# Kernel optimization log

Hardware: AMD Instinct MI355X
Metric: run time of the kernel (lower is better)

## Reference

```python
import jax, jax.numpy as jnp
import numpy as np

B, P, D, H, DH = 2, 2048, 1024, 16, 64
EPS = 1e-5

def layernorm(x, g, b):
    mu = jnp.mean(x, axis=-1, keepdims=True)
    var = jnp.mean((x - mu) ** 2, axis=-1, keepdims=True)
    return (x - mu) * jax.lax.rsqrt(var + EPS) * g + b

def setup_inputs() -> dict:
    key = jax.random.key(0)
    ks = jax.random.split(key, 16)
    s = lambda *sh: 1.0 / np.sqrt(sh[-2] if len(sh) > 1 else sh[-1])
    return {
        "x": jax.random.normal(ks[0], (B, P, D), jnp.float32),
        "Wq": jax.random.normal(ks[1], (H, D, DH), jnp.float32) / np.sqrt(D),
        "Wk": jax.random.normal(ks[2], (H, D, DH), jnp.float32) / np.sqrt(D),
        "Wv": jax.random.normal(ks[3], (H, D, DH), jnp.float32) / np.sqrt(D),
        "Wp": jax.random.normal(ks[4], (D, D), jnp.float32) / np.sqrt(D),
        "bp": jax.random.normal(ks[5], (D,), jnp.float32) * 0.01,
        "W1": jax.random.normal(ks[6], (D, 4 * D), jnp.float32) / np.sqrt(D),
        "b1": jax.random.normal(ks[7], (4 * D,), jnp.float32) * 0.01,
        "W2": jax.random.normal(ks[8], (4 * D, D), jnp.float32) / np.sqrt(4 * D),
        "b2": jax.random.normal(ks[9], (D,), jnp.float32) * 0.01,
        "g1": jnp.ones((D,), jnp.float32),
        "be1": jnp.zeros((D,), jnp.float32),
        "g2": jnp.ones((D,), jnp.float32),
        "be2": jnp.zeros((D,), jnp.float32),
    }

def reference(x, Wq, Wk, Wv, Wp, bp, W1, b1, W2, b2, g1, be1, g2, be2):
    Bb, Pp, Dd = x.shape
    h = layernorm(x, g1, be1)
    # per-head projections, stacked: [B,H,P,DH]
    q = jnp.einsum('bpd,hde->bhpe', h, Wq)
    k = jnp.einsum('bpd,hde->bhpe', h, Wk)
    v = jnp.einsum('bpd,hde->bhpe', h, Wv)
    # NOTE: source scales by dim_embd**-0.5 (C = x.shape[-1]), not dim_head
    scores = jnp.einsum('bhpe,bhqe->bhpq', q, k) * (Dd ** -0.5)
    mask = jnp.tril(jnp.ones((Pp, Pp), bool))
    scores = jnp.where(mask, scores, -jnp.inf)
    att = jax.nn.softmax(scores, axis=-1)
    o = jnp.einsum('bhpq,bhqe->bhpe', att, v)
    # concat heads: [B,P,H*DH]
    o = o.transpose(0, 2, 1, 3).reshape(Bb, Pp, -1)
    x = x + o @ Wp + bp
    h2 = layernorm(x, g2, be2)
    m = jax.nn.gelu(h2 @ W1 + b1, approximate=False)
    x = x + m @ W2 + b2
    return x
```

## Files before the change

### kernel.cpp

```cpp
#include <hip/hip_runtime.h>
#include <hip/hip_bf16.h>
#include <stdint.h>

typedef unsigned short u16;
typedef __attribute__((ext_vector_type(4))) float f32x4;
typedef __attribute__((ext_vector_type(8))) short bf16x8;
typedef __attribute__((ext_vector_type(4))) short bf16x4;
typedef __attribute__((ext_vector_type(4))) unsigned short u16x4;

static __device__ __forceinline__ u16 f2bf(float f) {
    union { float f; unsigned u; } v; v.f = f;
    unsigned r = v.u + 0x7fffu + ((v.u >> 16) & 1u);
    return (u16)(r >> 16);
}

static __device__ __forceinline__ void gload_lds16(const u16* g, u16* l) {
    __builtin_amdgcn_global_load_lds(
        (const __attribute__((address_space(1))) void*)(uintptr_t)g,
        (__attribute__((address_space(3))) void*)(uint32_t)(uintptr_t)l,
        16, 0, 0);
}

__global__ __launch_bounds__(256) void transpose_cast_b(
    const float* __restrict__ W, u16* __restrict__ out,
    int K, int N, long in_bs, long out_bs)
{
    __shared__ float tile[32][33];
    const float* Wb = W + (size_t)blockIdx.z * in_bs;
    u16* ob = out + (size_t)blockIdx.z * out_bs;
    int nt = blockIdx.x * 32, kt = blockIdx.y * 32;
    int tx = threadIdx.x & 31, ty = threadIdx.x >> 5;
    #pragma unroll
    for (int i = ty; i < 32; i += 8)
        tile[i][tx] = Wb[(size_t)(kt + i) * N + nt + tx];
    __syncthreads();
    #pragma unroll
    for (int i = ty; i < 32; i += 8)
        ob[(size_t)(nt + i) * K + kt + tx] = f2bf(tile[tx][i]);
}

__global__ __launch_bounds__(256) void ln_kernel(
    const float* __restrict__ x, const float* __restrict__ g,
    const float* __restrict__ be, u16* __restrict__ out)
{
    int row = blockIdx.x;
    int t = threadIdx.x;
    const float4* xr = (const float4*)(x + (size_t)row * 1024);
    float4 v = xr[t];
    float s = v.x + v.y + v.z + v.w;
    float sq = v.x * v.x + v.y * v.y + v.z * v.z + v.w * v.w;
    #pragma unroll
    for (int o = 1; o < 64; o <<= 1) {
        s  += __shfl_xor(s, o);
        sq += __shfl_xor(sq, o);
    }
    __shared__ float ps[4], pq[4];
    if ((t & 63) == 0) { ps[t >> 6] = s; pq[t >> 6] = sq; }
    __syncthreads();
    float S = ps[0] + ps[1] + ps[2] + ps[3];
    float Q = pq[0] + pq[1] + pq[2] + pq[3];
    float mu = S * (1.0f / 1024.0f);
    float var = Q * (1.0f / 1024.0f) - mu * mu;
    float rs = rsqrtf(var + 1e-5f);
    const float4 g4  = ((const float4*)g)[t];
    const float4 be4 = ((const float4*)be)[t];
    u16x4 o4;
    o4[0] = f2bf((v.x - mu) * rs * g4.x + be4.x);
    o4[1] = f2bf((v.y - mu) * rs * g4.y + be4.y);
    o4[2] = f2bf((v.z - mu) * rs * g4.z + be4.z);
    o4[3] = f2bf((v.w - mu) * rs * g4.w + be4.w);
    *(u16x4*)(out + (size_t)row * 1024 + t * 4) = o4;
}

template<int EPI>
__global__ __launch_bounds__(256) void gemm_bt(
    const u16* __restrict__ A, const u16* __restrict__ Bt,
    int M, int N, int K,
    const float* __restrict__ bias,
    void* __restrict__ Cout, u16* __restrict__ Kf, u16* __restrict__ Vf)
{
    __shared__ __align__(16) u16 SH[32768];
    const int bid = blockIdx.x;
    const int xcd = bid & 7, idx = bid >> 3;
    const int nmx = N >> 7;
    const int spx = (M >> 7) >> 3;
    const int tm = (xcd * spx + idx / nmx) * 128;
    const int tn = (idx % nmx) * 128;
    const int t = threadIdx.x;
    const int lane = t & 63, wave = t >> 6;
    const int wr = wave >> 1, wc = wave & 1;
    const int lq = lane & 15, lg = lane >> 4;
    f32x4 acc[4][4] = {};

    const int srow8 = lane >> 3;
    const int skoff = ((lane & 7) ^ srow8) * 8;
    const u16* ag = A  + (size_t)(tm + wave * 32 + srow8) * K + skoff;
    const u16* bg = Bt + (size_t)(tn + wave * 32 + srow8) * K + skoff;

    auto STAGE = [&](int buf, int k0) {
        u16* ab = SH + buf * 16384 + wave * 2048;
        u16* bb = SH + buf * 16384 + 8192 + wave * 2048;
        #pragma unroll
        for (int j = 0; j < 4; ++j) {
            gload_lds16(ag + (size_t)(j * 8) * K + k0, ab + j * 512);
            gload_lds16(bg + (size_t)(j * 8) * K + k0, bb + j * 512);
        }
    };

    const int KT = K >> 6;
    STAGE(0, 0);
    STAGE(1, 64);
    asm volatile("s_waitcnt vmcnt(8)" ::: "memory");
    __builtin_amdgcn_sched_barrier(0);
    __builtin_amdgcn_s_barrier();

    for (int kt = 0; kt < KT; ++kt) {
        const int buf = kt & 1;
        const u16* abuf = SH + buf * 16384;
        const u16* bbuf = abuf + 8192;
        bf16x8 af[4][2], bfv[4][2];
        #pragma unroll
        for (int m = 0; m < 4; ++m) {
            const int row = wr * 64 + m * 16 + lq;
            #pragma unroll
            for (int kk = 0; kk < 2; ++kk) {
                const int slot = (kk * 4 + lg) ^ (row & 7);
                af[m][kk] = *(const bf16x8*)(abuf + row * 64 + slot * 8);
            }
        }
        #pragma unroll
        for (int n = 0; n < 4; ++n) {
            const int col = wc * 64 + n * 16 + lq;
            #pragma unroll
            for (int kk = 0; kk < 2; ++kk) {
                const int slot = (kk * 4 + lg) ^ (col & 7);
                bfv[n][kk] = *(const bf16x8*)(bbuf + col * 64 + slot * 8);
            }
        }
        asm volatile("s_waitcnt lgkmcnt(0)" ::: "memory");
        __builtin_amdgcn_sched_barrier(0);
        __builtin_amdgcn_s_barrier();

        const bool pre = (kt + 2 < KT);
        if (pre) STAGE(buf, (kt + 2) << 6);

        __builtin_amdgcn_s_setprio(1);
        #pragma unroll
        for (int m = 0; m < 4; ++m)
            #pragma unroll
            for (int n = 0; n < 4; ++n)
                #pragma unroll
                for (int kk = 0; kk < 2; ++kk)
                    acc[m][n] = __builtin_amdgcn_mfma_f32_16x16x32_bf16(
                        af[m][kk], bfv[n][kk], acc[m][n], 0, 0, 0);
        __builtin_amdgcn_s_setprio(0);

        if (kt + 1 < KT) {
            if (pre) asm volatile("s_waitcnt vmcnt(8)" ::: "memory");
            else     asm volatile("s_waitcnt vmcnt(0)" ::: "memory");
            __builtin_amdgcn_sched_barrier(0);
            __builtin_amdgcn_s_barrier();
        }
    }

    if (EPI == 2 || (EPI == 3 && tn < 1024)) {
        __syncthreads();
        #pragma unroll
        for (int n = 0; n < 4; ++n) {
            const int cl = wc * 64 + n * 16 + lq;
            #pragma unroll
            for (int m = 0; m < 4; ++m) {
                const int rl = wr * 64 + m * 16 + lg * 4;
                #pragma unroll
                for (int r = 0; r < 4; ++r) {
                    float v = acc[m][n][r];
                    if (EPI == 2) {
                        float xx = v + bias[tn + cl];
                        v = 0.5f * xx * (1.0f + erff(xx * 0.70710678118654752f));
                    }
                    SH[(rl + r) * 136 + cl] = f2bf(v);
                }
            }
        }
        __syncthreads();
        const int row = t >> 1, half = t & 1;
        const int ncols = (EPI == 2) ? N : 1024;
        const uint4* srow4 = (const uint4*)(SH + row * 136 + half * 64);
        uint4* drow = (uint4*)((u16*)Cout + (size_t)(tm + row) * ncols + tn + half * 64);
        #pragma unroll
        for (int i = 0; i < 8; ++i)
            drow[i] = srow4[i];
    } else if (EPI == 3) {
        __syncthreads();
        const bool isK = (tn < 2048);
        #pragma unroll
        for (int n = 0; n < 4; ++n) {
            const int cl = wc * 64 + n * 16 + lq;
            const int d = cl & 63, hl = cl >> 6;
            #pragma unroll
            for (int m = 0; m < 4; ++m) {
                const int rl0 = wr * 64 + m * 16 + lg * 4;
                #pragma unroll
                for (int r = 0; r < 4; ++r) {
                    const int rl = rl0 + r;
                    const int p = rl & 63, kl = rl >> 6;
                    int off;
                    if (isK)
                        off = ((p >> 4) * 2 + (d >> 5)) * 512 + ((d >> 3) & 3) * 128
                            + (p & 15) * 8 + (d & 7);
                    else
                        off = ((p >> 4) * 4 + (d >> 4)) * 256 + ((p >> 2) & 3) * 64
                            + (d & 15) * 4 + (p & 3);
                    SH[(hl * 2 + kl) * 4096 + off] = f2bf(acc[m][n][r]);
                }
            }
        }
        __syncthreads();
        const int img = t >> 6, ln = t & 63;
        const int hl = img >> 1, kl = img & 1;
        const int hh = ((tn - (isK ? 1024 : 2048)) >> 6) + hl;
        const int bb = tm >> 11, pp = tm & 2047;
        u16* base = (isK ? Kf : Vf) + (size_t)(bb * 16 + hh) * 131072
                  + (size_t)((pp >> 6) + kl) * 4096;
        const u16* simg = SH + img * 4096;
        #pragma unroll
        for (int i = 0; i < 8; ++i)
            *(uint4*)(base + ln * 8 + i * 512) = *(const uint4*)(simg + ln * 8 + i * 512);
    }
}

__global__ __launch_bounds__(256) void gemm_bt64(
    const u16* __restrict__ A, const u16* __restrict__ Bt,
    int M, int N, int K,
    const float* __restrict__ bias, const float* __restrict__ res,
    float* __restrict__ Cout)
{
    __shared__ __align__(16) u16 SH[24576];
    const int bid = blockIdx.x;
    const int xcd = bid & 7, idx = bid >> 3;
    const int nmx = N >> 6;
    const int spx = (M >> 7) >> 3;
    const int tm = (xcd * spx + idx / nmx) * 128;
    const int tn = (idx % nmx) * 64;
    const int t = threadIdx.x;
    const int lane = t & 63, wave = t >> 6;
    const int wr = wave >> 1, wc = wave & 1;
    const int lq = lane & 15, lg = lane >> 4;
    f32x4 acc[4][2] = {};

    const int srow8 = lane >> 3;
    const int skoff = ((lane & 7) ^ srow8) * 8;
    const u16* ag = A  + (size_t)(tm + wave * 32 + srow8) * K + skoff;
    const u16* bg = Bt + (size_t)(tn + wave * 16 + srow8) * K + skoff;

    auto STAGE = [&](int buf, int k0) {
        u16* ab = SH + buf * 12288 + wave * 2048;
        u16* bb = SH + buf * 12288 + 8192 + wave * 1024;
        #pragma unroll
        for (int j = 0; j < 4; ++j)
            gload_lds16(ag + (size_t)(j * 8) * K + k0, ab + j * 512);
        #pragma unroll
        for (int j = 0; j < 2; ++j)
            gload_lds16(bg + (size_t)(j * 8) * K + k0, bb + j * 512);
    };

    const int KT = K >> 6;
    STAGE(0, 0);
    STAGE(1, 64);
    asm volatile("s_waitcnt vmcnt(6)" ::: "memory");
    __builtin_amdgcn_sched_barrier(0);
    __builtin_amdgcn_s_barrier();

    for (int kt = 0; kt < KT; ++kt) {
        const int buf = kt & 1;
        const u16* abuf = SH + buf * 12288;
        const u16* bbuf = abuf + 8192;
        bf16x8 af[4][2], bfr[2][2];
        #pragma unroll
        for (int m = 0; m < 4; ++m) {
            const int row = wr * 64 + m * 16 + lq;
            #pragma unroll
            for (int kk = 0; kk < 2; ++kk) {
                const int slot = (kk * 4 + lg) ^ (row & 7);
                af[m][kk] = *(const bf16x8*)(abuf + row * 64 + slot * 8);
            }
        }
        #pragma unroll
        for (int n = 0; n < 2; ++n) {
            const int col = wc * 32 + n * 16 + lq;
            #pragma unroll
            for (int kk = 0; kk < 2; ++kk) {
                const int slot = (kk * 4 + lg) ^ (col & 7);
                bfr[n][kk] = *(const bf16x8*)(bbuf + col * 64 + slot * 8);
            }
        }
        asm volatile("s_waitcnt lgkmcnt(0)" ::: "memory");
        __builtin_amdgcn_sched_barrier(0);
        __builtin_amdgcn_s_barrier();

        const bool pre = (kt + 2 < KT);
        if (pre) STAGE(buf, (kt + 2) << 6);

        __builtin_amdgcn_s_setprio(1);
        #pragma unroll
        for (int m = 0; m < 4; ++m)
            #pragma unroll
            for (int n = 0; n < 2; ++n)
                #pragma unroll
                for (int kk = 0; kk < 2; ++kk)
                    acc[m][n] = __builtin_amdgcn_mfma_f32_16x16x32_bf16(
                        af[m][kk], bfr[n][kk], acc[m][n], 0, 0, 0);
        __builtin_amdgcn_s_setprio(0);

        if (kt + 1 < KT) {
            if (pre) asm volatile("s_waitcnt vmcnt(6)" ::: "memory");
            else     asm volatile("s_waitcnt vmcnt(0)" ::: "memory");
            __builtin_amdgcn_sched_barrier(0);
            __builtin_amdgcn_s_barrier();
        }
    }

    #pragma unroll
    for (int m = 0; m < 4; ++m)
        #pragma unroll
        for (int n = 0; n < 2; ++n) {
            const int col = tn + wc * 32 + n * 16 + lq;
            #pragma unroll
            for (int r = 0; r < 4; ++r) {
                const int row = tm + wr * 64 + m * 16 + lg * 4 + r;
                Cout[(size_t)row * N + col] = acc[m][n][r] + bias[col] + res[(size_t)row * N + col];
            }
        }
}

__global__ __launch_bounds__(256, 4) void attn_kernel(
    const u16* __restrict__ qb, const u16* __restrict__ Kf,
    const u16* __restrict__ Vf, u16* __restrict__ o)
{
    const int P = 2048;
    __shared__ __align__(16) u16 KB[2][4096];
    __shared__ __align__(16) u16 VB[2][4096];
    int blk = blockIdx.x;
    int qt = 31 - (blk >> 5);
    int bh = blk & 31;
    int h = bh & 15, b = bh >> 4;
    int w = threadIdx.x >> 6, lane = threadIdx.x & 63;
    int lq = lane & 15, lg = lane >> 4;
    int q0 = qt * 64 + w * 16;
    const u16* qptr = qb + (size_t)(b * P + q0 + lq) * 1024 + h * 64 + lg * 8;
    bf16x8 qf0 = *(const bf16x8*)qptr;
    bf16x8 qf1 = *(const bf16x8*)(qptr + 32);
    const u16* Kfb = Kf + (size_t)bh * 131072;
    const u16* Vfb = Vf + (size_t)bh * 131072;
    const float C2 = 0.03125f * 1.44269504f;
    const int moff = w * 16 + lq;
    float m2 = -1e30f, l_run = 0.f;
    f32x4 accO[4] = {};
    const int nkvb = qt + 1;

    const int vsel = w >> 1, half = w & 1;
    auto STAGE = [&](int buf, int kvb) {
        const u16* src = (vsel ? Vfb : Kfb) + (size_t)kvb * 4096 + half * 2048 + lane * 8;
        u16* dst = (vsel ? &VB[buf][half * 2048] : &KB[buf][half * 2048]);
        #pragma unroll
        for (int i = 0; i < 4; ++i)
            gload_lds16(src + i * 512, dst + i * 512);
    };

    auto COMPUTE = [&](int buf, bool last) {
        const u16* kbase = KB[buf] + lane * 8;
        f32x4 st[4];
        #pragma unroll
        for (int ss = 0; ss < 4; ++ss) {
            bf16x8 kf0 = *(const bf16x8*)(kbase + ss * 1024);
            bf16x8 kf1 = *(const bf16x8*)(kbase + ss * 1024 + 512);
            f32x4 z = {0.f, 0.f, 0.f, 0.f};
            st[ss] = __builtin_amdgcn_mfma_f32_16x16x32_bf16(kf0, qf0, z, 0, 0, 0);
            st[ss] = __builtin_amdgcn_mfma_f32_16x16x32_bf16(kf1, qf1, st[ss], 0, 0, 0);
        }
        float rmax = -1e30f;
        #pragma unroll
        for (int ss = 0; ss < 4; ++ss)
            #pragma unroll
            for (int r = 0; r < 4; ++r) {
                float v = st[ss][r] * C2;
                if (last && (ss * 16 + lg * 4 + r > moff)) v = -1e30f;
                st[ss][r] = v;
                rmax = fmaxf(rmax, v);
            }
        rmax = fmaxf(rmax, __shfl_xor(rmax, 16));
        rmax = fmaxf(rmax, __shfl_xor(rmax, 32));
        if (__any(rmax > m2 + 11.5f)) {
            float m2n = fmaxf(m2, rmax);
            float alpha = exp2f(m2 - m2n);
            l_run *= alpha;
            #pragma unroll
            for (int r = 0; r < 4; ++r) {
                float ar = __shfl(alpha, lg * 4 + r);
                accO[0][r] *= ar; accO[1][r] *= ar; accO[2][r] *= ar; accO[3][r] *= ar;
            }
            m2 = m2n;
        }
        float psum = 0.f;
        bf16x4 pf[4];
        #pragma unroll
        for (int ss = 0; ss < 4; ++ss)
            #pragma unroll
            for (int r = 0; r < 4; ++r) {
                float pv = exp2f(st[ss][r] - m2);
                psum += pv;
                pf[ss][r] = (short)f2bf(pv);
            }
        psum += __shfl_xor(psum, 16);
        psum += __shfl_xor(psum, 32);
        l_run += psum;
        const u16* vbase = VB[buf] + lane * 4;
        #pragma unroll
        for (int ks = 0; ks < 4; ++ks)
            #pragma unroll
            for (int c = 0; c < 4; ++c) {
                bf16x4 vfr = *(const bf16x4*)(vbase + (ks * 4 + c) * 256);
                accO[c] = __builtin_amdgcn_mfma_f32_16x16x16bf16_1k(pf[ks], vfr, accO[c], 0, 0, 0);
            }
    };

    STAGE(0, 0);
    __syncthreads();
    int cur = 0;
    for (int kvb = 0; kvb < nkvb; ++kvb) {
        if (kvb + 1 < nkvb) STAGE(cur ^ 1, kvb + 1);
        COMPUTE(cur, kvb == nkvb - 1);
        __syncthreads();
        cur ^= 1;
    }

    #pragma unroll
    for (int r = 0; r < 4; ++r) {
        float l_r = __shfl(l_run, lg * 4 + r);
        float inv = 1.0f / l_r;
        size_t orow = (size_t)(b * P + q0 + lg * 4 + r) * 1024 + h * 64;
        #pragma unroll
        for (int c = 0; c < 4; ++c)
            o[orow + c * 16 + lq] = f2bf(accO[c][r] * inv);
    }
}

extern "C" void kernel_launch(void* const* d_in, const int* in_sizes, int n_in,
                              void* d_out, int out_size, void* d_ws, size_t ws_size,
                              hipStream_t stream)
{
    const float* x   = (const float*)d_in[0];
    const float* Wq  = (const float*)d_in[1];
    const float* Wk  = (const float*)d_in[2];
    const float* Wv  = (const float*)d_in[3];
    const float* Wp  = (const float*)d_in[4];
    const float* bp  = (const float*)d_in[5];
    const float* W1  = (const float*)d_in[6];
    const float* b1  = (const float*)d_in[7];
    const float* W2  = (const float*)d_in[8];
    const float* b2  = (const float*)d_in[9];
    const float* g1  = (const float*)d_in[10];
    const float* be1 = (const float*)d_in[11];
    const float* g2  = (const float*)d_in[12];
    const float* be2 = (const float*)d_in[13];

    char* ws = (char*)d_ws;
    u16*  h     = (u16*)(ws + 0);
    u16*  qbuf  = (u16*)(ws + 8388608);
    u16*  Kf    = (u16*)(ws + 16777216);
    u16*  Vf    = (u16*)(ws + 25165824);
    u16*  o     = (u16*)(ws + 33554432);
    float* x1   = (float*)(ws + 41943040);
    u16*  wqkvT = (u16*)(ws + 58720256);
    u16*  wpT   = (u16*)(ws + 65011712);
    u16*  w1T   = (u16*)(ws + 67108864);
    u16*  w2T   = (u16*)(ws + 75497472);
    u16*  m     = (u16*)(ws + 0);
    u16*  h2    = o;
    float* out  = (float*)d_out;

    transpose_cast_b<<<dim3(2, 32, 16), 256, 0, stream>>>(Wq, wqkvT,           1024, 64, 65536, 65536);
    transpose_cast_b<<<dim3(2, 32, 16), 256, 0, stream>>>(Wk, wqkvT + 1048576, 1024, 64, 65536, 65536);
    transpose_cast_b<<<dim3(2, 32, 16), 256, 0, stream>>>(Wv, wqkvT + 2097152, 1024, 64, 65536, 65536);
    transpose_cast_b<<<dim3(32, 32, 1), 256, 0, stream>>>(Wp, wpT, 1024, 1024, 0, 0);
    transpose_cast_b<<<dim3(128, 32, 1), 256, 0, stream>>>(W1, w1T, 1024, 4096, 0, 0);
    transpose_cast_b<<<dim3(32, 128, 1), 256, 0, stream>>>(W2, w2T, 4096, 1024, 0, 0);

    ln_kernel<<<4096, 256, 0, stream>>>(x, g1, be1, h);
    gemm_bt<3><<<768, 256, 0, stream>>>(h, wqkvT, 4096, 3072, 1024, nullptr, qbuf, Kf, Vf);
    attn_kernel<<<1024, 256, 0, stream>>>(qbuf, Kf, Vf, o);
    gemm_bt64<<<512, 256, 0, stream>>>(o, wpT, 4096, 1024, 1024, bp, x, x1);
    ln_kernel<<<4096, 256, 0, stream>>>(x1, g2, be2, h2);
    gemm_bt<2><<<1024, 256, 0, stream>>>(h2, w1T, 4096, 4096, 1024, b1, m, nullptr, nullptr);
    gemm_bt64<<<512, 256, 0, stream>>>(m, w2T, 4096, 1024, 4096, b2, x1, out);
}
```

Before: 238.2 us.

## Replace 128x128 GEMM with 256x256-tile 512-thread kernel for QKV and FC1

The QKV projection and FC1 GEMMs move from 128x128 tiles with 4 waves to 256x256 tiles with 8 waves. Each wave computes 128x64 in two halves, reusing its B fragments across both. The larger tile raises arithmetic intensity and halves global/LDS traffic per FLOP. In exchange it uses 128KB of LDS with one block per CU and a simpler single-stage-ahead prefetch. The grids become 192 and 256 blocks, which may leave CUs idle on a 256-CU part and loses the XCD-aware block remapping.

```diff
diff --git a/kernel.cpp b/kernel.cpp
--- a/kernel.cpp
+++ b/kernel.cpp
@@ -73,77 +73,69 @@
 }
 
 template<int EPI>
-__global__ __launch_bounds__(256) void gemm_bt(
+__global__ __launch_bounds__(512, 1) void gemm256(
     const u16* __restrict__ A, const u16* __restrict__ Bt,
     int M, int N, int K,
     const float* __restrict__ bias,
     void* __restrict__ Cout, u16* __restrict__ Kf, u16* __restrict__ Vf)
 {
-    __shared__ __align__(16) u16 SH[32768];
-    const int bid = blockIdx.x;
-    const int xcd = bid & 7, idx = bid >> 3;
-    const int nmx = N >> 7;
-    const int spx = (M >> 7) >> 3;
-    const int tm = (xcd * spx + idx / nmx) * 128;
-    const int tn = (idx % nmx) * 128;
+    __shared__ __align__(16) u16 SH[65536];
+    const int tm = blockIdx.y * 256, tn = blockIdx.x * 256;
     const int t = threadIdx.x;
-    const int lane = t & 63, wave = t >> 6;
-    const int wr = wave >> 1, wc = wave & 1;
+    const int lane = t & 63, w = t >> 6;
+    const int wm = w >> 2, wn = w & 3;
     const int lq = lane & 15, lg = lane >> 4;
-    f32x4 acc[4][4] = {};
+    f32x4 acc[8][4] = {};
 
     const int srow8 = lane >> 3;
     const int skoff = ((lane & 7) ^ srow8) * 8;
-    const u16* ag = A  + (size_t)(tm + wave * 32 + srow8) * K + skoff;
-    const u16* bg = Bt + (size_t)(tn + wave * 32 + srow8) * K + skoff;
+    const u16* ag = A  + (size_t)(tm + w * 32 + srow8) * K + skoff;
+    const u16* bg = Bt + (size_t)(tn + w * 32 + srow8) * K + skoff;
 
     auto STAGE = [&](int buf, int k0) {
-        u16* ab = SH + buf * 16384 + wave * 2048;
-        u16* bb = SH + buf * 16384 + 8192 + wave * 2048;
+        u16* ab = SH + buf * 32768 + w * 2048;
+        u16* bb = SH + buf * 32768 + 16384 + w * 2048;
         #pragma unroll
         for (int j = 0; j < 4; ++j) {
             gload_lds16(ag + (size_t)(j * 8) * K + k0, ab + j * 512);
             gload_lds16(bg + (size_t)(j * 8) * K + k0, bb + j * 512);
         }
     };
+    auto LDA = [&](bf16x8 (*af)[2], int buf, int a0) {
+        #pragma unroll
+        for (int m = 0; m < 4; ++m) {
+            const int row = wm * 128 + a0 + m * 16 + lq;
+            #pragma unroll
+            for (int kk = 0; kk < 2; ++kk) {
+                const int slot = (kk * 4 + lg) ^ (row & 7);
+                af[m][kk] = *(const bf16x8*)(SH + buf * 32768 + row * 64 + slot * 8);
+            }
+        }
+    };
 
     const int KT = K >> 6;
     STAGE(0, 0);
-    STAGE(1, 64);
-    asm volatile("s_waitcnt vmcnt(8)" ::: "memory");
+    asm volatile("s_waitcnt vmcnt(0)" ::: "memory");
     __builtin_amdgcn_sched_barrier(0);
     __builtin_amdgcn_s_barrier();
 
     for (int kt = 0; kt < KT; ++kt) {
         const int buf = kt & 1;
-        const u16* abuf = SH + buf * 16384;
-        const u16* bbuf = abuf + 8192;
+        const bool nxt = (kt + 1 < KT);
+        if (nxt) STAGE(buf ^ 1, (kt + 1) << 6);
         bf16x8 af[4][2], bfv[4][2];
         #pragma unroll
-        for (int m = 0; m < 4; ++m) {
-            const int row = wr * 64 + m * 16 + lq;
-            #pragma unroll
-            for (int kk = 0; kk < 2; ++kk) {
-                const int slot = (kk * 4 + lg) ^ (row & 7);
-                af[m][kk] = *(const bf16x8*)(abuf + row * 64 + slot * 8);
-            }
-        }
-        #pragma unroll
         for (int n = 0; n < 4; ++n) {
-            const int col = wc * 64 + n * 16 + lq;
+            const int col = wn * 64 + n * 16 + lq;
             #pragma unroll
             for (int kk = 0; kk < 2; ++kk) {
                 const int slot = (kk * 4 + lg) ^ (col & 7);
-                bfv[n][kk] = *(const bf16x8*)(bbuf + col * 64 + slot * 8);
-            }
-        }
+                bfv[n][kk] = *(const bf16x8*)(SH + buf * 32768 + 16384 + col * 64 + slot * 8);
+            }
+        }
+        LDA(af, buf, 0);
         asm volatile("s_waitcnt lgkmcnt(0)" ::: "memory");
         __builtin_amdgcn_sched_barrier(0);
-        __builtin_amdgcn_s_barrier();
-
-        const bool pre = (kt + 2 < KT);
-        if (pre) STAGE(buf, (kt + 2) << 6);
-
         __builtin_amdgcn_s_setprio(1);
         #pragma unroll
         for (int m = 0; m < 4; ++m)
@@ -154,52 +146,69 @@
                     acc[m][n] = __builtin_amdgcn_mfma_f32_16x16x32_bf16(
                         af[m][kk], bfv[n][kk], acc[m][n], 0, 0, 0);
         __builtin_amdgcn_s_setprio(0);
-
-        if (kt + 1 < KT) {
-            if (pre) asm volatile("s_waitcnt vmcnt(8)" ::: "memory");
-            else     asm volatile("s_waitcnt vmcnt(0)" ::: "memory");
+        LDA(af, buf, 64);
+        asm volatile("s_waitcnt lgkmcnt(0)" ::: "memory");
+        __builtin_amdgcn_sched_barrier(0);
+        __builtin_amdgcn_s_setprio(1);
+        #pragma unroll
+        for (int m = 0; m < 4; ++m)
+            #pragma unroll
+            for (int n = 0; n < 4; ++n)
+                #pragma unroll
+                for (int kk = 0; kk < 2; ++kk)
+                    acc[4 + m][n] = __builtin_amdgcn_mfma_f32_16x16x32_bf16(
+                        af[m][kk], bfv[n][kk], acc[4 + m][n], 0, 0, 0);
+        __builtin_amdgcn_s_setprio(0);
+        if (nxt) {
+            asm volatile("s_waitcnt vmcnt(0)" ::: "memory");
             __builtin_amdgcn_sched_barrier(0);
-            __builtin_amdgcn_s_barrier();
-        }
+        }
+        __builtin_amdgcn_s_barrier();
     }
 
     if (EPI == 2 || (EPI == 3 && tn < 1024)) {
         __syncthreads();
-        #pragma unroll
-        for (int n = 0; n < 4; ++n) {
-            const int cl = wc * 64 + n * 16 + lq;
-            #pragma unroll
-            for (int m = 0; m < 4; ++m) {
-                const int rl = wr * 64 + m * 16 + lg * 4;
+        const int ncols = (EPI == 2) ? N : 1024;
+        #pragma unroll
+        for (int rh = 0; rh < 2; ++rh) {
+            if (rh) __syncthreads();
+            if (wm == rh) {
                 #pragma unroll
-                for (int r = 0; r < 4; ++r) {
-                    float v = acc[m][n][r];
-                    if (EPI == 2) {
-                        float xx = v + bias[tn + cl];
-                        v = 0.5f * xx * (1.0f + erff(xx * 0.70710678118654752f));
+                for (int n = 0; n < 4; ++n) {
+                    const int cl = wn * 64 + n * 16 + lq;
+                    #pragma unroll
+                    for (int m = 0; m < 8; ++m) {
+                        const int rl = m * 16 + lg * 4;
+                        #pragma unroll
+                        for (int r = 0; r < 4; ++r) {
+                            float v = acc[m][n][r];
+                            if (EPI == 2) {
+                                float xx = v + bias[tn + cl];
+                                v = 0.5f * xx * (1.0f + erff(xx * 0.70710678118654752f));
+                            }
+                            SH[(rl + r) * 264 + cl] = f2bf(v);
+                        }
                     }
-                    SH[(rl + r) * 136 + cl] = f2bf(v);
                 }
             }
-        }
-        __syncthreads();
-        const int row = t >> 1, half = t & 1;
-        const int ncols = (EPI == 2) ? N : 1024;
-        const uint4* srow4 = (const uint4*)(SH + row * 136 + half * 64);
-        uint4* drow = (uint4*)((u16*)Cout + (size_t)(tm + row) * ncols + tn + half * 64);
-        #pragma unroll
-        for (int i = 0; i < 8; ++i)
-            drow[i] = srow4[i];
+            __syncthreads();
+            const int row = t >> 2, q = t & 3;
+            const uint4* srow4 = (const uint4*)(SH + row * 264 + q * 64);
+            uint4* drow = (uint4*)((u16*)Cout + (size_t)(tm + rh * 128 + row) * ncols + tn + q * 64);
+            #pragma unroll
+            for (int i = 0; i < 8; ++i)
+                drow[i] = srow4[i];
+        }
     } else if (EPI == 3) {
         __syncthreads();
         const bool isK = (tn < 2048);
         #pragma unroll
         for (int n = 0; n < 4; ++n) {
-            const int cl = wc * 64 + n * 16 + lq;
+            const int cl = wn * 64 + n * 16 + lq;
             const int d = cl & 63, hl = cl >> 6;
             #pragma unroll
-            for (int m = 0; m < 4; ++m) {
-                const int rl0 = wr * 64 + m * 16 + lg * 4;
+            for (int m = 0; m < 8; ++m) {
+                const int rl0 = wm * 128 + m * 16 + lg * 4;
                 #pragma unroll
                 for (int r = 0; r < 4; ++r) {
                     const int rl = rl0 + r;
@@ -211,21 +220,21 @@
                     else
                         off = ((p >> 4) * 4 + (d >> 4)) * 256 + ((p >> 2) & 3) * 64
                             + (d & 15) * 4 + (p & 3);
-                    SH[(hl * 2 + kl) * 4096 + off] = f2bf(acc[m][n][r]);
+                    SH[(hl * 4 + kl) * 4096 + off] = f2bf(acc[m][n][r]);
                 }
             }
         }
         __syncthreads();
-        const int img = t >> 6, ln = t & 63;
-        const int hl = img >> 1, kl = img & 1;
+        const int img = t >> 5, ln = t & 31;
+        const int hl = img >> 2, kl = img & 3;
         const int hh = ((tn - (isK ? 1024 : 2048)) >> 6) + hl;
         const int bb = tm >> 11, pp = tm & 2047;
         u16* base = (isK ? Kf : Vf) + (size_t)(bb * 16 + hh) * 131072
                   + (size_t)((pp >> 6) + kl) * 4096;
         const u16* simg = SH + img * 4096;
         #pragma unroll
-        for (int i = 0; i < 8; ++i)
-            *(uint4*)(base + ln * 8 + i * 512) = *(const uint4*)(simg + ln * 8 + i * 512);
+        for (int i = 0; i < 16; ++i)
+            *(uint4*)(base + ln * 8 + i * 256) = *(const uint4*)(simg + ln * 8 + i * 256);
     }
 }
 
@@ -487,10 +496,10 @@
     transpose_cast_b<<<dim3(32, 128, 1), 256, 0, stream>>>(W2, w2T, 4096, 1024, 0, 0);
 
     ln_kernel<<<4096, 256, 0, stream>>>(x, g1, be1, h);
-    gemm_bt<3><<<768, 256, 0, stream>>>(h, wqkvT, 4096, 3072, 1024, nullptr, qbuf, Kf, Vf);
+    gemm256<3><<<dim3(12, 16), 512, 0, stream>>>(h, wqkvT, 4096, 3072, 1024, nullptr, qbuf, Kf, Vf);
     attn_kernel<<<1024, 256, 0, stream>>>(qbuf, Kf, Vf, o);
     gemm_bt64<<<512, 256, 0, stream>>>(o, wpT, 4096, 1024, 1024, bp, x, x1);
     ln_kernel<<<4096, 256, 0, stream>>>(x1, g2, be2, h2);
-    gemm_bt<2><<<1024, 256, 0, stream>>>(h2, w1T, 4096, 4096, 1024, b1, m, nullptr, nullptr);
+    gemm256<2><<<dim3(16, 16), 512, 0, stream>>>(h2, w1T, 4096, 4096, 1024, b1, m, nullptr, nullptr);
     gemm_bt64<<<512, 256, 0, stream>>>(m, w2T, 4096, 1024, 4096, b2, x1, out);
 }
```

New measurement: 384.9 us. +61.6%, slower.
